# Optimization experiments

Hardware: AMD Instinct MI355X
Metric: run time of the kernel (lower is better)

The kernel has to match this reference:

```python
import jax, jax.numpy as jnp
import numpy as np
import math

N_NODES = 50000
N_EDGES = 10000
NNZ = 800000
F_IN = 128
NHID = 128
F_OUT = 64
N_LAYERS = 2
ALPHA = 0.1
LAMDA = 0.5


def setup_inputs() -> dict:
    key = jax.random.key(0)
    ks = jax.random.split(key, 8)
    x = jax.random.normal(ks[0], (N_NODES, F_IN), dtype=jnp.float32)
    vertex = jax.random.randint(ks[1], (NNZ,), 0, N_NODES, dtype=jnp.int32)
    edges = jax.random.randint(ks[2], (NNZ,), 0, N_EDGES, dtype=jnp.int32)
    # parameters (Kaiming-ish scaling)
    W0 = jax.random.normal(ks[3], (F_IN, NHID), dtype=jnp.float32) / np.sqrt(F_IN)
    b0 = jnp.zeros((NHID,), dtype=jnp.float32)
    Ws = jax.random.normal(ks[4], (N_LAYERS, NHID, NHID), dtype=jnp.float32) / np.sqrt(NHID)
    Wout = jax.random.normal(ks[5], (NHID, F_OUT), dtype=jnp.float32) / np.sqrt(NHID)
    bout = jnp.zeros((F_OUT,), dtype=jnp.float32)
    return {"x": x, "W0": W0, "b0": b0, "Ws": Ws, "Wout": Wout,
            "bout": bout, "vertex": vertex, "edges": edges}


def _scatter_mean(src, index, num_segments):
    # src: [nnz, d]; index: [nnz] -> out: [num_segments, d]
    s = jax.ops.segment_sum(src, index, num_segments=num_segments)
    cnt = jax.ops.segment_sum(jnp.ones((src.shape[0],), src.dtype), index,
                              num_segments=num_segments)
    return s / jnp.maximum(cnt, 1.0)[:, None]


def _normalize_l2(X):
    # UniGNN normalize_l2: detached row norm, inf->0 scale
    norm = jax.lax.stop_gradient(jnp.linalg.norm(X, axis=-1, keepdims=True))
    scale = jnp.where(norm > 0, 1.0 / jnp.maximum(norm, 1e-30), 0.0)
    return X * scale


def reference(x, W0, b0, Ws, Wout, bout, vertex, edges):
    x = jax.nn.relu(x @ W0 + b0)          # input Linear + ReLU
    x0 = x
    Xe = None
    for i in range(N_LAYERS):
        beta = math.log(LAMDA / (i + 1) + 1.0)
        Xve = x[vertex]                    # [nnz, nhid] vertex->incidence gather
        Xe = _scatter_mean(Xve, edges, N_EDGES)    # [E, nhid]
        Xev = Xe[edges]                    # [nnz, nhid] edge->incidence gather
        Xv = _scatter_mean(Xev, vertex, N_NODES)   # [N, nhid]
        X = _normalize_l2(Xv)
        Xi = (1.0 - ALPHA) * X + ALPHA * x0
        x = (1.0 - beta) * Xi + beta * (Xi @ Ws[i])
        x = jax.nn.relu(x)
    out = x @ Wout + bout
    return (out, Xe)
```

## Files before the change

kernel.cpp:

```cpp
#include <hip/hip_runtime.h>
#include <hip/hip_bf16.h>
#include <math.h>

#define NODES 50000
#define EDGES 10000
#define NNZ   800000
#define FIN   128
#define NHID  128
#define FOUT  64

#define NHB    128
#define SLICE  (NNZ / NHB)
#define VHALF  25000
#define VWORDS (VHALF / 2)

#define WCONV_BLOCKS 128
#define GEMM_BLOCKS  ((NODES + 63) / 64)
#define EDGE_BLOCKS  (EDGES * 64 / 256)
#define NF_BLOCKS    (NODES / 16)

typedef __attribute__((ext_vector_type(8))) short bf16x8;
typedef __attribute__((ext_vector_type(4))) float f32x4;
typedef unsigned short ushort_t;
typedef unsigned int uint_t;

__device__ __forceinline__ ushort_t f2b(float f) {
    __hip_bfloat16 h = __float2bfloat16(f);
    return *reinterpret_cast<ushort_t*>(&h);
}
__device__ __forceinline__ float u2f(unsigned u) {
    union { unsigned u; float f; } c; c.u = u; return c.f;
}
__device__ __forceinline__ float us2f(ushort_t u) { return u2f((unsigned)u << 16); }
__device__ __forceinline__ unsigned pk2(float lo, float hi) {
    return (unsigned)f2b(lo) | ((unsigned)f2b(hi) << 16);
}

__global__ __launch_bounds__(256)
void hist_wconv_kernel(const int* __restrict__ vertex, const int* __restrict__ edges,
                       uint_t* __restrict__ cbe, uint_t* __restrict__ cbv,
                       const float* __restrict__ W0, const float* __restrict__ Ws,
                       const float* __restrict__ Wout,
                       ushort_t* __restrict__ Wt0, ushort_t* __restrict__ WsT,
                       ushort_t* __restrict__ WoutT) {
    __shared__ uint_t lds_u[VWORDS];
    const int t = threadIdx.x;
    if (blockIdx.x < NHB) {
        const int b = blockIdx.x;
        for (int k = t; k < EDGES; k += 256) lds_u[k] = 0;
        __syncthreads();
        const int base = b * SLICE;
        for (int i = base + t; i < base + SLICE; i += 256)
            atomicAdd(&lds_u[edges[i]], 1u);
        __syncthreads();
        for (int k = t; k < EDGES; k += 256) cbe[b * EDGES + k] = lds_u[k];
    } else if (blockIdx.x < NHB + 2 * NHB) {
        const int hb = blockIdx.x - NHB, h = hb >> 7, bs = hb & 127;
        for (int w = t; w < VWORDS; w += 256) lds_u[w] = 0;
        __syncthreads();
        const int base = bs * SLICE, voff = h * VHALF;
        for (int i = base + t; i < base + SLICE; i += 256) {
            const int vk = vertex[i] - voff;
            if ((unsigned)vk < (unsigned)VHALF)
                atomicAdd(&lds_u[vk >> 1], 1u << ((vk & 1) * 16));
        }
        __syncthreads();
        for (int w = t; w < VWORDS; w += 256) cbv[hb * VWORDS + w] = lds_u[w];
    } else {
        const int i = (blockIdx.x - 3 * NHB) * 256 + t;
        if (i < 128 * 128) { int c = i >> 7, k = i & 127; Wt0[c * 128 + k] = f2b(W0[k * 128 + c]); }
        if (i < 2 * 128 * 128) {
            int l = i >> 14, r = i & 16383, c = r >> 7, k = r & 127;
            WsT[l * 16384 + c * 128 + k] = f2b(Ws[l * 16384 + k * 128 + c]);
        }
        if (i < 64 * 128) { int c = i >> 7, k = i & 127; WoutT[c * 128 + k] = f2b(Wout[k * 64 + c]); }
    }
}

__global__ __launch_bounds__(256)
void colscan_kernel(uint_t* __restrict__ cbe, uint_t* __restrict__ cbv,
                    int* __restrict__ cnt_e, int* __restrict__ cnt_v) {
    const int flat = blockIdx.x * 256 + threadIdx.x;
    if (flat < EDGES) {
        uint_t sum = 0;
        for (int b = 0; b < NHB; ++b) {
            uint_t* p = &cbe[b * EDGES + flat];
            const uint_t tv = *p; *p = sum; sum += tv;
        }
        cnt_e[flat] = (int)sum;
    } else if (flat < EDGES + 2 * VWORDS) {
        const int idx = flat - EDGES, h = idx / VWORDS, w = idx % VWORDS;
        uint_t s0 = 0, s1 = 0;
        for (int bs = 0; bs < NHB; ++bs) {
            uint_t* p = &cbv[(h * NHB + bs) * VWORDS + w];
            const uint_t u = *p; *p = s0 | (s1 << 16);
            s0 += u & 0xffffu; s1 += u >> 16;
        }
        cnt_v[h * VHALF + 2 * w]     = (int)s0;
        cnt_v[h * VHALF + 2 * w + 1] = (int)s1;
    }
}

__device__ __forceinline__ void scan_impl(const int* __restrict__ cnt, int* __restrict__ rp,
                                          const int n) {
    __shared__ int wsum[16];
    __shared__ int carry_sh;
    const int t = threadIdx.x, lane = t & 63, w = t >> 6;
    if (t == 0) carry_sh = 0;
    __syncthreads();
    for (int base = 0; base < n; base += 8192) {
        const int idx = base + t * 8;
        int v[8];
        if (idx + 8 <= n) {
            const int4 a = *(const int4*)(cnt + idx);
            const int4 b = *(const int4*)(cnt + idx + 4);
            v[0] = a.x; v[1] = a.y; v[2] = a.z; v[3] = a.w;
            v[4] = b.x; v[5] = b.y; v[6] = b.z; v[7] = b.w;
        } else {
#pragma unroll
            for (int j = 0; j < 8; ++j) v[j] = (idx + j < n) ? cnt[idx + j] : 0;
        }
        int sum8 = 0;
#pragma unroll
        for (int j = 0; j < 8; ++j) sum8 += v[j];
        int x = sum8;
#pragma unroll
        for (int o = 1; o < 64; o <<= 1) {
            int y = __shfl_up(x, o);
            if (lane >= o) x += y;
        }
        if (lane == 63) wsum[w] = x;
        __syncthreads();
        if (t < 16) {
            int s = wsum[t];
#pragma unroll
            for (int o = 1; o < 16; o <<= 1) {
                int y = __shfl_up(s, o);
                if (t >= o) s += y;
            }
            wsum[t] = s;
        }
        __syncthreads();
        const int carry = carry_sh;
        int pre = carry + (x - sum8) + (w ? wsum[w - 1] : 0);
        if (idx < n) {
#pragma unroll
            for (int j = 0; j < 8; ++j)
                if (idx + j < n) { rp[idx + j] = pre; pre += v[j]; }
        }
        __syncthreads();
        if (t == 1023) carry_sh = carry + wsum[15];
        __syncthreads();
    }
    if (t == 0) rp[n] = carry_sh;
}

__global__ __launch_bounds__(1024)
void scan2_kernel(const int* __restrict__ cnt_e, int* __restrict__ rp_e,
                  const int* __restrict__ cnt_v, int* __restrict__ rp_v) {
    if (blockIdx.x == 0) scan_impl(cnt_e, rp_e, EDGES);
    else                 scan_impl(cnt_v, rp_v, NODES);
}

__global__ __launch_bounds__(256)
void fill_gemm_kernel(const int* __restrict__ vertex, const int* __restrict__ edges,
                      const uint_t* __restrict__ cbe, const uint_t* __restrict__ cbv,
                      const int* __restrict__ rp_e, const int* __restrict__ rp_v,
                      int* __restrict__ col_e, int* __restrict__ col_v,
                      const float* __restrict__ X, const ushort_t* __restrict__ Wt,
                      const float* __restrict__ bias, ushort_t* __restrict__ x0) {
    __shared__ uint_t lds_u[VWORDS];
    const int t = threadIdx.x;
    if (blockIdx.x < NHB) {
        const int b = blockIdx.x;
        for (int k = t; k < EDGES; k += 256)
            lds_u[k] = (uint_t)rp_e[k] + cbe[b * EDGES + k];
        __syncthreads();
        const int base = b * SLICE;
        for (int i = base + t; i < base + SLICE; i += 256) {
            const int e = edges[i], v = vertex[i];
            const uint_t pos = atomicAdd(&lds_u[e], 1u);
            col_e[pos] = v;
        }
        return;
    }
    if (blockIdx.x < 3 * NHB) {
        const int fb = blockIdx.x - NHB, h = fb >> 7, bs = fb & 127;
        for (int w = t; w < VWORDS; w += 256) lds_u[w] = cbv[fb * VWORDS + w];
        __syncthreads();
        const int base = bs * SLICE, voff = h * VHALF;
        for (int i = base + t; i < base + SLICE; i += 256) {
            const int v = vertex[i];
            const int vk = v - voff;
            if ((unsigned)vk < (unsigned)VHALF) {
                const int e = edges[i];
                const uint_t sh = (uint_t)(vk & 1) * 16;
                const uint_t old = atomicAdd(&lds_u[vk >> 1], 1u << sh);
                col_v[rp_v[v] + (int)((old >> sh) & 0xffffu)] = e;
            }
        }
        return;
    }
    const int lane = threadIdx.x & 63, wave = threadIdx.x >> 6;
    const int row0 = (blockIdx.x - 3 * NHB) * 64 + wave * 16;
    if (row0 >= NODES) return;
    const int r = lane & 15, kb = lane >> 4;
    const int row = row0 + r;
    bf16x8 a[4];
#pragma unroll
    for (int k0 = 0; k0 < 4; ++k0) {
        const float* p = X + (size_t)row * FIN + k0 * 32 + kb * 8;
        const float4 lo = *(const float4*)p;
        const float4 hi = *(const float4*)(p + 4);
        bf16x8 tt;
        tt[0] = f2b(lo.x); tt[1] = f2b(lo.y); tt[2] = f2b(lo.z); tt[3] = f2b(lo.w);
        tt[4] = f2b(hi.x); tt[5] = f2b(hi.y); tt[6] = f2b(hi.z); tt[7] = f2b(hi.w);
        a[k0] = tt;
    }
    f32x4 acc[8];
#pragma unroll
    for (int c0 = 0; c0 < 8; ++c0) {
        const float bv = bias[c0 * 16 + r];
        acc[c0] = (f32x4){bv, bv, bv, bv};
    }
#pragma unroll
    for (int k0 = 0; k0 < 4; ++k0)
#pragma unroll
        for (int c0 = 0; c0 < 8; ++c0) {
            const bf16x8 b = *(const bf16x8*)(Wt + (size_t)(c0 * 16 + r) * FIN + k0 * 32 + kb * 8);
            acc[c0] = __builtin_amdgcn_mfma_f32_16x16x32_bf16(a[k0], b, acc[c0], 0, 0, 0);
        }
#pragma unroll
    for (int c0 = 0; c0 < 8; ++c0) {
        const int col = c0 * 16 + r;
#pragma unroll
        for (int v = 0; v < 4; ++v) {
            const int orow = row0 + kb * 4 + v;
            float val = acc[c0][v];
            val = val > 0.f ? val : 0.f;
            x0[(size_t)orow * NHID + col] = f2b(val);
        }
    }
}

__global__ __launch_bounds__(256)
void edge_gather_kernel(const ushort_t* __restrict__ x, const int* __restrict__ rp,
                        const int* __restrict__ ci, ushort_t* __restrict__ Xe,
                        float* __restrict__ out_xe) {
    const int e = (blockIdx.x * 256 + (int)threadIdx.x) >> 6;
    if (e >= EDGES) return;
    const int lane = threadIdx.x & 63;
    const int sub = lane >> 4, lr = lane & 15;
    const int beg = rp[e], end = rp[e + 1];
    float a[8] = {};
    for (int base = beg; base < end; base += 64) {
        const int m = min(64, end - base);
        const int idx_l = (lane < m) ? ci[base + lane] : 0;
        const int steps = (m + 3) >> 2;
#pragma unroll 4
        for (int j = 0; j < steps; ++j) {
            const int slot = j * 4 + sub;
            const int src = __shfl(idx_l, slot);
            if (slot < m) {
                const uint4 d = *(const uint4*)(x + (size_t)src * NHID + lr * 8);
                a[0] += u2f(d.x << 16); a[1] += u2f(d.x & 0xffff0000u);
                a[2] += u2f(d.y << 16); a[3] += u2f(d.y & 0xffff0000u);
                a[4] += u2f(d.z << 16); a[5] += u2f(d.z & 0xffff0000u);
                a[6] += u2f(d.w << 16); a[7] += u2f(d.w & 0xffff0000u);
            }
        }
    }
#pragma unroll
    for (int k = 0; k < 8; ++k) {
        a[k] += __shfl_xor(a[k], 16);
        a[k] += __shfl_xor(a[k], 32);
    }
    const float inv = 1.f / (float)max(end - beg, 1);
    if (sub == 0) {
        float vv[8];
#pragma unroll
        for (int k = 0; k < 8; ++k) vv[k] = a[k] * inv;
        uint4 o;
        o.x = pk2(vv[0], vv[1]); o.y = pk2(vv[2], vv[3]);
        o.z = pk2(vv[4], vv[5]); o.w = pk2(vv[6], vv[7]);
        *(uint4*)(Xe + (size_t)e * NHID + lr * 8) = o;
        if (out_xe) {
            const float4 f0 = {vv[0], vv[1], vv[2], vv[3]};
            const float4 f1 = {vv[4], vv[5], vv[6], vv[7]};
            *(float4*)(out_xe + (size_t)e * NHID + lr * 8) = f0;
            *(float4*)(out_xe + (size_t)e * NHID + lr * 8 + 4) = f1;
        }
    }
}

__device__ __forceinline__ void node_phase1(const ushort_t* __restrict__ Xe,
                                            const int* __restrict__ rp,
                                            const int* __restrict__ ci,
                                            const ushort_t* __restrict__ x0,
                                            const int vbase,
                                            ushort_t* __restrict__ xl) {
    const int lane = threadIdx.x & 63, wave = threadIdx.x >> 6;
    const int sub = lane >> 4, lr = lane & 15;
    const int row = wave * 4 + sub;
    const int v = vbase + row;
    const int beg = rp[v], end = rp[v + 1];
    const int sbase = lane & 48;
    float a[8] = {};
    for (int base = beg; base < end; base += 16) {
        const int m = min(16, end - base);
        const int idx_l = (lr < m) ? ci[base + lr] : 0;
#pragma unroll 4
        for (int j = 0; j < m; ++j) {
            const int src = __shfl(idx_l, sbase + j);
            const uint4 d = *(const uint4*)(Xe + (size_t)src * NHID + lr * 8);
            a[0] += u2f(d.x << 16); a[1] += u2f(d.x & 0xffff0000u);
            a[2] += u2f(d.y << 16); a[3] += u2f(d.y & 0xffff0000u);
            a[4] += u2f(d.z << 16); a[5] += u2f(d.z & 0xffff0000u);
            a[6] += u2f(d.w << 16); a[7] += u2f(d.w & 0xffff0000u);
        }
    }
    const float inv = 1.f / (float)max(end - beg, 1);
    float mk[8], s = 0.f;
#pragma unroll
    for (int k = 0; k < 8; ++k) { mk[k] = a[k] * inv; s += mk[k] * mk[k]; }
    s += __shfl_xor(s, 1); s += __shfl_xor(s, 2);
    s += __shfl_xor(s, 4); s += __shfl_xor(s, 8);
    const float norm = sqrtf(s);
    const float scale = norm > 0.f ? 1.f / fmaxf(norm, 1e-30f) : 0.f;
    const uint4 u0 = *(const uint4*)(x0 + (size_t)v * NHID + lr * 8);
    float xv[8];
    xv[0] = u2f(u0.x << 16); xv[1] = u2f(u0.x & 0xffff0000u);
    xv[2] = u2f(u0.y << 16); xv[3] = u2f(u0.y & 0xffff0000u);
    xv[4] = u2f(u0.z << 16); xv[5] = u2f(u0.z & 0xffff0000u);
    xv[6] = u2f(u0.w << 16); xv[7] = u2f(u0.w & 0xffff0000u);
    float o[8];
#pragma unroll
    for (int k = 0; k < 8; ++k) o[k] = 0.9f * mk[k] * scale + 0.1f * xv[k];
    uint4 ou;
    ou.x = pk2(o[0], o[1]); ou.y = pk2(o[2], o[3]);
    ou.z = pk2(o[4], o[5]); ou.w = pk2(o[6], o[7]);
    *(uint4*)(xl + row * 136 + lr * 8) = ou;
}

__global__ __launch_bounds__(256)
void node_l1_kernel(const ushort_t* __restrict__ Xe, const int* __restrict__ rp,
                    const int* __restrict__ ci, const ushort_t* __restrict__ x0,
                    const ushort_t* __restrict__ Wt, float beta,
                    ushort_t* __restrict__ xout) {
    __shared__ ushort_t xl[16 * 136];
    const int vbase = blockIdx.x * 16;
    node_phase1(Xe, rp, ci, x0, vbase, xl);
    __syncthreads();
    const int lane = threadIdx.x & 63, wave = threadIdx.x >> 6;
    const int r = lane & 15, kb = lane >> 4;
    bf16x8 a2[4];
#pragma unroll
    for (int k0 = 0; k0 < 4; ++k0)
        a2[k0] = *(const bf16x8*)(xl + r * 136 + k0 * 32 + kb * 8);
    f32x4 acc[2] = {};
#pragma unroll
    for (int k0 = 0; k0 < 4; ++k0)
#pragma unroll
        for (int cc = 0; cc < 2; ++cc) {
            const int c0 = wave * 2 + cc;
            const bf16x8 b = *(const bf16x8*)(Wt + (size_t)(c0 * 16 + r) * NHID + k0 * 32 + kb * 8);
            acc[cc] = __builtin_amdgcn_mfma_f32_16x16x32_bf16(a2[k0], b, acc[cc], 0, 0, 0);
        }
    const float xim = 1.f - beta;
#pragma unroll
    for (int cc = 0; cc < 2; ++cc) {
        const int col = (wave * 2 + cc) * 16 + r;
#pragma unroll
        for (int v = 0; v < 4; ++v) {
            const int row = kb * 4 + v;
            const float xi = us2f(xl[row * 136 + col]);
            float val = xim * xi + beta * acc[cc][v];
            val = val > 0.f ? val : 0.f;
            xout[(size_t)(vbase + row) * NHID + col] = f2b(val);
        }
    }
}

__global__ __launch_bounds__(256)
void node_l2_out_kernel(const ushort_t* __restrict__ Xe, const int* __restrict__ rp,
                        const int* __restrict__ ci, const ushort_t* __restrict__ x0,
                        const ushort_t* __restrict__ Wt, const ushort_t* __restrict__ WoT,
                        const float* __restrict__ bias, float beta,
                        float* __restrict__ out) {
    __shared__ ushort_t xl[16 * 136];
    __shared__ ushort_t x2[16 * 136];
    const int vbase = blockIdx.x * 16;
    node_phase1(Xe, rp, ci, x0, vbase, xl);
    __syncthreads();
    const int lane = threadIdx.x & 63, wave = threadIdx.x >> 6;
    const int r = lane & 15, kb = lane >> 4;
    {
        bf16x8 a2[4];
#pragma unroll
        for (int k0 = 0; k0 < 4; ++k0)
            a2[k0] = *(const bf16x8*)(xl + r * 136 + k0 * 32 + kb * 8);
        f32x4 acc[2] = {};
#pragma unroll
        for (int k0 = 0; k0 < 4; ++k0)
#pragma unroll
            for (int cc = 0; cc < 2; ++cc) {
                const int c0 = wave * 2 + cc;
                const bf16x8 b = *(const bf16x8*)(Wt + (size_t)(c0 * 16 + r) * NHID + k0 * 32 + kb * 8);
                acc[cc] = __builtin_amdgcn_mfma_f32_16x16x32_bf16(a2[k0], b, acc[cc], 0, 0, 0);
            }
        const float xim = 1.f - beta;
#pragma unroll
        for (int cc = 0; cc < 2; ++cc) {
            const int col = (wave * 2 + cc) * 16 + r;
#pragma unroll
            for (int v = 0; v < 4; ++v) {
                const int row = kb * 4 + v;
                const float xi = us2f(xl[row * 136 + col]);
                float val = xim * xi + beta * acc[cc][v];
                val = val > 0.f ? val : 0.f;
                x2[row * 136 + col] = f2b(val);
            }
        }
    }
    __syncthreads();
    bf16x8 a3[4];
#pragma unroll
    for (int k0 = 0; k0 < 4; ++k0)
        a3[k0] = *(const bf16x8*)(x2 + r * 136 + k0 * 32 + kb * 8);
    const float bv = bias[wave * 16 + r];
    f32x4 facc = (f32x4){bv, bv, bv, bv};
#pragma unroll
    for (int k0 = 0; k0 < 4; ++k0) {
        const bf16x8 b = *(const bf16x8*)(WoT + (size_t)(wave * 16 + r) * NHID + k0 * 32 + kb * 8);
        facc = __builtin_amdgcn_mfma_f32_16x16x32_bf16(a3[k0], b, facc, 0, 0, 0);
    }
#pragma unroll
    for (int v = 0; v < 4; ++v) {
        const int row = kb * 4 + v;
        out[(size_t)(vbase + row) * FOUT + wave * 16 + r] = facc[v];
    }
}

extern "C" void kernel_launch(void* const* d_in, const int* in_sizes, int n_in,
                              void* d_out, int out_size, void* d_ws, size_t ws_size,
                              hipStream_t stream) {
    const float* x_in  = (const float*)d_in[0];
    const float* W0    = (const float*)d_in[1];
    const float* b0    = (const float*)d_in[2];
    const float* Ws    = (const float*)d_in[3];
    const float* Wout  = (const float*)d_in[4];
    const float* bout  = (const float*)d_in[5];
    const int* vertex  = (const int*)d_in[6];
    const int* edges   = (const int*)d_in[7];

    ushort_t* Xe   = (ushort_t*)d_ws;
    ushort_t* x    = Xe + (size_t)EDGES * NHID;
    ushort_t* x0   = x  + (size_t)NODES * NHID;
    ushort_t* Wt0  = x0 + (size_t)NODES * NHID;
    ushort_t* WsT  = Wt0 + 128 * 128;
    ushort_t* WoutT= WsT + 2 * 128 * 128;
    int* cnt_e = (int*)(WoutT + 64 * 128);
    int* cnt_v = cnt_e + EDGES;
    int* rp_e  = cnt_v + NODES;
    int* rp_v  = rp_e + EDGES + 4;
    uint_t* cbe = (uint_t*)(rp_v + NODES + 4);
    uint_t* cbv = cbe + (size_t)NHB * EDGES;
    int* col_e = (int*)(cbv + (size_t)2 * NHB * VWORDS);
    int* col_v = col_e + NNZ;

    float* out    = (float*)d_out;
    float* out_xe = out + (size_t)NODES * FOUT;

    hist_wconv_kernel<<<3 * NHB + WCONV_BLOCKS, 256, 0, stream>>>(
        vertex, edges, cbe, cbv, W0, Ws, Wout, Wt0, WsT, WoutT);
    colscan_kernel<<<(EDGES + 2 * VWORDS + 255) / 256, 256, 0, stream>>>(
        cbe, cbv, cnt_e, cnt_v);
    scan2_kernel<<<2, 1024, 0, stream>>>(cnt_e, rp_e, cnt_v, rp_v);
    fill_gemm_kernel<<<3 * NHB + GEMM_BLOCKS, 256, 0, stream>>>(
        vertex, edges, cbe, cbv, rp_e, rp_v, col_e, col_v, x_in, Wt0, b0, x0);

    const float betas[2] = {logf(1.5f), logf(1.25f)};

    edge_gather_kernel<<<EDGE_BLOCKS, 256, 0, stream>>>(x0, rp_e, col_e, Xe, (float*)nullptr);
    node_l1_kernel<<<NF_BLOCKS, 256, 0, stream>>>(Xe, rp_v, col_v, x0, WsT, betas[0], x);
    edge_gather_kernel<<<EDGE_BLOCKS, 256, 0, stream>>>(x, rp_e, col_e, Xe, out_xe);
    node_l2_out_kernel<<<NF_BLOCKS, 256, 0, stream>>>(
        Xe, rp_v, col_v, x0, WsT + (size_t)NHID * NHID, WoutT, bout, betas[1], out);
}
```

Baseline: 213.4 us.

## Pack CSR column indices and edge histograms into 16-bit, split vertex histogram into quarters

Column index arrays for both CSR structures are now stored as 16-bit values. Edge histogram counts are packed two per 32-bit word, and the vertex histogram is split into four quarter ranges instead of two halves, which shrinks LDS per block and changes the block counts. The aim is less index bandwidth in the gather kernels and better occupancy in the histogram and fill kernels. The trade-off is more blocks each rescanning the full nnz slice, and a reliance on vertex ids below 65536 and per-bin slice counts below 65536, which holds for these sizes.

```diff
diff --git a/kernel.cpp b/kernel.cpp
--- a/kernel.cpp
+++ b/kernel.cpp
@@ -9,10 +9,11 @@
 #define NHID  128
 #define FOUT  64
 
-#define NHB    128
-#define SLICE  (NNZ / NHB)
-#define VHALF  25000
-#define VWORDS (VHALF / 2)
+#define NHB      128
+#define SLICE    (NNZ / NHB)
+#define EWORDS   (EDGES / 2)
+#define VQUARTER 12500
+#define QWORDS   (VQUARTER / 2)
 
 #define WCONV_BLOCKS 128
 #define GEMM_BLOCKS  ((NODES + 63) / 64)
@@ -43,31 +44,33 @@
                        const float* __restrict__ Wout,
                        ushort_t* __restrict__ Wt0, ushort_t* __restrict__ WsT,
                        ushort_t* __restrict__ WoutT) {
-    __shared__ uint_t lds_u[VWORDS];
+    __shared__ uint_t lds_u[QWORDS];
     const int t = threadIdx.x;
     if (blockIdx.x < NHB) {
         const int b = blockIdx.x;
-        for (int k = t; k < EDGES; k += 256) lds_u[k] = 0;
+        for (int w = t; w < EWORDS; w += 256) lds_u[w] = 0;
         __syncthreads();
         const int base = b * SLICE;
-        for (int i = base + t; i < base + SLICE; i += 256)
-            atomicAdd(&lds_u[edges[i]], 1u);
-        __syncthreads();
-        for (int k = t; k < EDGES; k += 256) cbe[b * EDGES + k] = lds_u[k];
-    } else if (blockIdx.x < NHB + 2 * NHB) {
-        const int hb = blockIdx.x - NHB, h = hb >> 7, bs = hb & 127;
-        for (int w = t; w < VWORDS; w += 256) lds_u[w] = 0;
-        __syncthreads();
-        const int base = bs * SLICE, voff = h * VHALF;
+        for (int i = base + t; i < base + SLICE; i += 256) {
+            const int e = edges[i];
+            atomicAdd(&lds_u[e >> 1], 1u << ((e & 1) * 16));
+        }
+        __syncthreads();
+        for (int w = t; w < EWORDS; w += 256) cbe[b * EWORDS + w] = lds_u[w];
+    } else if (blockIdx.x < NHB + 4 * NHB) {
+        const int qb = blockIdx.x - NHB, q = qb >> 7, bs = qb & 127;
+        for (int w = t; w < QWORDS; w += 256) lds_u[w] = 0;
+        __syncthreads();
+        const int base = bs * SLICE, voff = q * VQUARTER;
         for (int i = base + t; i < base + SLICE; i += 256) {
             const int vk = vertex[i] - voff;
-            if ((unsigned)vk < (unsigned)VHALF)
+            if ((unsigned)vk < (unsigned)VQUARTER)
                 atomicAdd(&lds_u[vk >> 1], 1u << ((vk & 1) * 16));
         }
         __syncthreads();
-        for (int w = t; w < VWORDS; w += 256) cbv[hb * VWORDS + w] = lds_u[w];
+        for (int w = t; w < QWORDS; w += 256) cbv[qb * QWORDS + w] = lds_u[w];
     } else {
-        const int i = (blockIdx.x - 3 * NHB) * 256 + t;
+        const int i = (blockIdx.x - 5 * NHB) * 256 + t;
         if (i < 128 * 128) { int c = i >> 7, k = i & 127; Wt0[c * 128 + k] = f2b(W0[k * 128 + c]); }
         if (i < 2 * 128 * 128) {
             int l = i >> 14, r = i & 16383, c = r >> 7, k = r & 127;
@@ -81,23 +84,25 @@
 void colscan_kernel(uint_t* __restrict__ cbe, uint_t* __restrict__ cbv,
                     int* __restrict__ cnt_e, int* __restrict__ cnt_v) {
     const int flat = blockIdx.x * 256 + threadIdx.x;
-    if (flat < EDGES) {
-        uint_t sum = 0;
+    if (flat < EWORDS) {
+        uint_t s0 = 0, s1 = 0;
         for (int b = 0; b < NHB; ++b) {
-            uint_t* p = &cbe[b * EDGES + flat];
-            const uint_t tv = *p; *p = sum; sum += tv;
-        }
-        cnt_e[flat] = (int)sum;
-    } else if (flat < EDGES + 2 * VWORDS) {
-        const int idx = flat - EDGES, h = idx / VWORDS, w = idx % VWORDS;
+            uint_t* p = &cbe[b * EWORDS + flat];
+            const uint_t u = *p; *p = s0 | (s1 << 16);
+            s0 += u & 0xffffu; s1 += u >> 16;
+        }
+        cnt_e[2 * flat]     = (int)s0;
+        cnt_e[2 * flat + 1] = (int)s1;
+    } else if (flat < EWORDS + 4 * QWORDS) {
+        const int idx = flat - EWORDS, q = idx / QWORDS, w = idx % QWORDS;
         uint_t s0 = 0, s1 = 0;
         for (int bs = 0; bs < NHB; ++bs) {
-            uint_t* p = &cbv[(h * NHB + bs) * VWORDS + w];
+            uint_t* p = &cbv[(q * NHB + bs) * QWORDS + w];
             const uint_t u = *p; *p = s0 | (s1 << 16);
             s0 += u & 0xffffu; s1 += u >> 16;
         }
-        cnt_v[h * VHALF + 2 * w]     = (int)s0;
-        cnt_v[h * VHALF + 2 * w + 1] = (int)s1;
+        cnt_v[q * VQUARTER + 2 * w]     = (int)s0;
+        cnt_v[q * VQUARTER + 2 * w + 1] = (int)s1;
     }
 }
 
@@ -166,43 +171,43 @@
 void fill_gemm_kernel(const int* __restrict__ vertex, const int* __restrict__ edges,
                       const uint_t* __restrict__ cbe, const uint_t* __restrict__ cbv,
                       const int* __restrict__ rp_e, const int* __restrict__ rp_v,
-                      int* __restrict__ col_e, int* __restrict__ col_v,
+                      ushort_t* __restrict__ col_e, ushort_t* __restrict__ col_v,
                       const float* __restrict__ X, const ushort_t* __restrict__ Wt,
                       const float* __restrict__ bias, ushort_t* __restrict__ x0) {
-    __shared__ uint_t lds_u[VWORDS];
+    __shared__ uint_t lds_u[QWORDS];
     const int t = threadIdx.x;
     if (blockIdx.x < NHB) {
         const int b = blockIdx.x;
-        for (int k = t; k < EDGES; k += 256)
-            lds_u[k] = (uint_t)rp_e[k] + cbe[b * EDGES + k];
+        for (int w = t; w < EWORDS; w += 256) lds_u[w] = cbe[b * EWORDS + w];
         __syncthreads();
         const int base = b * SLICE;
         for (int i = base + t; i < base + SLICE; i += 256) {
             const int e = edges[i], v = vertex[i];
-            const uint_t pos = atomicAdd(&lds_u[e], 1u);
-            col_e[pos] = v;
+            const uint_t sh = (uint_t)(e & 1) * 16;
+            const uint_t old = atomicAdd(&lds_u[e >> 1], 1u << sh);
+            col_e[rp_e[e] + (int)((old >> sh) & 0xffffu)] = (ushort_t)v;
         }
         return;
     }
-    if (blockIdx.x < 3 * NHB) {
-        const int fb = blockIdx.x - NHB, h = fb >> 7, bs = fb & 127;
-        for (int w = t; w < VWORDS; w += 256) lds_u[w] = cbv[fb * VWORDS + w];
-        __syncthreads();
-        const int base = bs * SLICE, voff = h * VHALF;
+    if (blockIdx.x < 5 * NHB) {
+        const int qb = blockIdx.x - NHB, q = qb >> 7, bs = qb & 127;
+        for (int w = t; w < QWORDS; w += 256) lds_u[w] = cbv[qb * QWORDS + w];
+        __syncthreads();
+        const int base = bs * SLICE, voff = q * VQUARTER;
         for (int i = base + t; i < base + SLICE; i += 256) {
             const int v = vertex[i];
             const int vk = v - voff;
-            if ((unsigned)vk < (unsigned)VHALF) {
+            if ((unsigned)vk < (unsigned)VQUARTER) {
                 const int e = edges[i];
                 const uint_t sh = (uint_t)(vk & 1) * 16;
                 const uint_t old = atomicAdd(&lds_u[vk >> 1], 1u << sh);
-                col_v[rp_v[v] + (int)((old >> sh) & 0xffffu)] = e;
+                col_v[rp_v[v] + (int)((old >> sh) & 0xffffu)] = (ushort_t)e;
             }
         }
         return;
     }
     const int lane = threadIdx.x & 63, wave = threadIdx.x >> 6;
-    const int row0 = (blockIdx.x - 3 * NHB) * 64 + wave * 16;
+    const int row0 = (blockIdx.x - 5 * NHB) * 64 + wave * 16;
     if (row0 >= NODES) return;
     const int r = lane & 15, kb = lane >> 4;
     const int row = row0 + r;
@@ -245,7 +250,7 @@
 
 __global__ __launch_bounds__(256)
 void edge_gather_kernel(const ushort_t* __restrict__ x, const int* __restrict__ rp,
-                        const int* __restrict__ ci, ushort_t* __restrict__ Xe,
+                        const ushort_t* __restrict__ ci, ushort_t* __restrict__ Xe,
                         float* __restrict__ out_xe) {
     const int e = (blockIdx.x * 256 + (int)threadIdx.x) >> 6;
     if (e >= EDGES) return;
@@ -255,7 +260,7 @@
     float a[8] = {};
     for (int base = beg; base < end; base += 64) {
         const int m = min(64, end - base);
-        const int idx_l = (lane < m) ? ci[base + lane] : 0;
+        const int idx_l = (lane < m) ? (int)ci[base + lane] : 0;
         const int steps = (m + 3) >> 2;
 #pragma unroll 4
         for (int j = 0; j < steps; ++j) {
@@ -295,7 +300,7 @@
 
 __device__ __forceinline__ void node_phase1(const ushort_t* __restrict__ Xe,
                                             const int* __restrict__ rp,
-                                            const int* __restrict__ ci,
+                                            const ushort_t* __restrict__ ci,
                                             const ushort_t* __restrict__ x0,
                                             const int vbase,
                                             ushort_t* __restrict__ xl) {
@@ -308,7 +313,7 @@
     float a[8] = {};
     for (int base = beg; base < end; base += 16) {
         const int m = min(16, end - base);
-        const int idx_l = (lr < m) ? ci[base + lr] : 0;
+        const int idx_l = (lr < m) ? (int)ci[base + lr] : 0;
 #pragma unroll 4
         for (int j = 0; j < m; ++j) {
             const int src = __shfl(idx_l, sbase + j);
@@ -344,7 +349,7 @@
 
 __global__ __launch_bounds__(256)
 void node_l1_kernel(const ushort_t* __restrict__ Xe, const int* __restrict__ rp,
-                    const int* __restrict__ ci, const ushort_t* __restrict__ x0,
+                    const ushort_t* __restrict__ ci, const ushort_t* __restrict__ x0,
                     const ushort_t* __restrict__ Wt, float beta,
                     ushort_t* __restrict__ xout) {
     __shared__ ushort_t xl[16 * 136];
@@ -383,7 +388,7 @@
 
 __global__ __launch_bounds__(256)
 void node_l2_out_kernel(const ushort_t* __restrict__ Xe, const int* __restrict__ rp,
-                        const int* __restrict__ ci, const ushort_t* __restrict__ x0,
+                        const ushort_t* __restrict__ ci, const ushort_t* __restrict__ x0,
                         const ushort_t* __restrict__ Wt, const ushort_t* __restrict__ WoT,
                         const float* __restrict__ bias, float beta,
                         float* __restrict__ out) {
@@ -464,19 +469,19 @@
     int* rp_e  = cnt_v + NODES;
     int* rp_v  = rp_e + EDGES + 4;
     uint_t* cbe = (uint_t*)(rp_v + NODES + 4);
-    uint_t* cbv = cbe + (size_t)NHB * EDGES;
-    int* col_e = (int*)(cbv + (size_t)2 * NHB * VWORDS);
-    int* col_v = col_e + NNZ;
+    uint_t* cbv = cbe + (size_t)NHB * EWORDS;
+    ushort_t* col_e = (ushort_t*)(cbv + (size_t)4 * NHB * QWORDS);
+    ushort_t* col_v = col_e + NNZ;
 
     float* out    = (float*)d_out;
     float* out_xe = out + (size_t)NODES * FOUT;
 
-    hist_wconv_kernel<<<3 * NHB + WCONV_BLOCKS, 256, 0, stream>>>(
+    hist_wconv_kernel<<<5 * NHB + WCONV_BLOCKS, 256, 0, stream>>>(
         vertex, edges, cbe, cbv, W0, Ws, Wout, Wt0, WsT, WoutT);
-    colscan_kernel<<<(EDGES + 2 * VWORDS + 255) / 256, 256, 0, stream>>>(
+    colscan_kernel<<<(EWORDS + 4 * QWORDS + 255) / 256, 256, 0, stream>>>(
         cbe, cbv, cnt_e, cnt_v);
     scan2_kernel<<<2, 1024, 0, stream>>>(cnt_e, rp_e, cnt_v, rp_v);
-    fill_gemm_kernel<<<3 * NHB + GEMM_BLOCKS, 256, 0, stream>>>(
+    fill_gemm_kernel<<<5 * NHB + GEMM_BLOCKS, 256, 0, stream>>>(
         vertex, edges, cbe, cbv, rp_e, rp_v, col_e, col_v, x_in, Wt0, b0, x0);
 
     const float betas[2] = {logf(1.5f), logf(1.25f)};
```

Result: no change. 211.2 us (-1.0%).
